# Kernel optimization log

Hardware: AMD Instinct MI355X
Metric: run time of the kernel (lower is better)

Reference implementation:

```python
import jax, jax.numpy as jnp
import numpy as np

N_E, E_DIM, BETA = 8192, 512, 0.25


def setup_inputs() -> dict:
    key = jax.random.key(0)
    k1, k2 = jax.random.split(key)
    z = jax.random.normal(k1, (16, 1024, E_DIM), dtype=jnp.float32)
    # embedding initialized uniform(-1/n_e, 1/n_e)
    emb_w = jax.random.uniform(k2, (N_E, E_DIM), dtype=jnp.float32,
                               minval=-1.0 / N_E, maxval=1.0 / N_E)
    return {"z": z, "emb_w": emb_w}


def reference(z, emb_w):
    B, T, D = z.shape
    zf = z.reshape(-1, D)  # [BT, D]
    # squared-distance matrix: ||z||^2 + ||e||^2 - 2 z e^T  -> [BT, n_e]
    d = (jnp.sum(zf * zf, axis=1, keepdims=True)
         + jnp.sum(emb_w * emb_w, axis=1)
         - 2.0 * jnp.einsum('bd,nd->bn', zf, emb_w))
    idx = jnp.argmin(d, axis=1)  # [BT]
    z_q = emb_w[idx].reshape(z.shape)  # [B, T, D]
    # legacy=False: beta * commit + codebook term
    loss = (BETA * jnp.mean((jax.lax.stop_gradient(z_q) - z) ** 2)
            + jnp.mean((z_q - jax.lax.stop_gradient(z)) ** 2))
    # straight-through: value equals z_q
    z_q_st = z + jax.lax.stop_gradient(z_q - z)
    idx_out = idx.reshape(B, T)
    v = jnp.var(idx_out.astype(jnp.float32))
    return z_q_st, loss, idx_out, v
```

## Files before the change

### kernel.cpp

```cpp
#include <hip/hip_runtime.h>


#define BT   16384
#define DIMS 512
#define NE   8192
#define NSPLIT 8
#define NTPB (NE / NSPLIT / 128)

#define LOSS_OFF 8388608
#define IDX_OFF  8388609
#define V_OFF    8404993

#define BEST_OFF  0
#define ENORM_OFF 131072
#define SUMS_OFF  163840
#define CNT_OFF   163864

typedef __attribute__((ext_vector_type(8))) short short8;
typedef __attribute__((ext_vector_type(4))) float floatx4;

#define AS1(p) ((const __attribute__((address_space(1))) void*)(p))
#define AS3(p) ((__attribute__((address_space(3))) void*)(p))

__device__ __forceinline__ unsigned f2bf(float f) {
    unsigned u = __builtin_bit_cast(unsigned, f);
    u += 0x7FFFu + ((u >> 16) & 1u);
    return u >> 16;
}

__global__ __launch_bounds__(256) void prep_kernel(
    const float* __restrict__ z, const float* __restrict__ emb,
    ushort* __restrict__ zh, ushort* __restrict__ ehh,
    float* __restrict__ enorm, unsigned long long* __restrict__ best,
    double* __restrict__ sums, unsigned* __restrict__ counter)
{
    const int lane = threadIdx.x & 63, w = threadIdx.x >> 6;
    const int b = blockIdx.x;
    if (b < NE / 4) {
        const int row = b * 4 + w;
        const float4* p = (const float4*)(emb + (size_t)row * DIMS + lane * 8);
        float4 a = p[0], bb = p[1];
        uint4 h;
        h.x = f2bf(a.x) | (f2bf(a.y) << 16);
        h.y = f2bf(a.z) | (f2bf(a.w) << 16);
        h.z = f2bf(bb.x) | (f2bf(bb.y) << 16);
        h.w = f2bf(bb.z) | (f2bf(bb.w) << 16);
        *(uint4*)(ehh + (size_t)row * DIMS + lane * 8) = h;
        float s = a.x*a.x + a.y*a.y + a.z*a.z + a.w*a.w
                + bb.x*bb.x + bb.y*bb.y + bb.z*bb.z + bb.w*bb.w;
        #pragma unroll
        for (int off = 32; off > 0; off >>= 1) s += __shfl_down(s, off, 64);
        if (lane == 0) enorm[row] = s;
    } else {
        const int row = (b - NE / 4) * 4 + w;
        const float4* p = (const float4*)(z + (size_t)row * DIMS + lane * 8);
        float4 a = p[0], bb = p[1];
        uint4 h;
        h.x = f2bf(a.x) | (f2bf(a.y) << 16);
        h.y = f2bf(a.z) | (f2bf(a.w) << 16);
        h.z = f2bf(bb.x) | (f2bf(bb.y) << 16);
        h.w = f2bf(bb.z) | (f2bf(bb.w) << 16);
        *(uint4*)(zh + (size_t)row * DIMS + lane * 8) = h;
    }
    const int gid = b * 256 + threadIdx.x;
    if (gid < BT) best[gid] = 0xFFFFFFFFFFFFFFFFULL;
    if (gid == 0) { sums[0] = 0.0; sums[1] = 0.0; sums[2] = 0.0; *counter = 0u; }
}

__global__ __launch_bounds__(256) void argmin_mfma(
    const ushort* __restrict__ zh, const ushort* __restrict__ eh,
    const float* __restrict__ enorm, unsigned long long* __restrict__ best)
{
    __shared__ __align__(16) ushort lds[2][128][64];
    const int t = threadIdx.x;
    const int w = t >> 6, lane = t & 63;
    const int quad = lane >> 4, l15 = lane & 15;
    const int mt = blockIdx.x & 127, ns = blockIdx.x >> 7;
    const int m0 = mt * 128;
    const int wm = (w & 1) * 64, wn = (w >> 1) * 64;

    const int half = w & 1;
    const int tile = (w < 2) ? 0 : 1;
    const int srow = half * 64 + (lane >> 3);
    const int lchunk = (lane & 7) ^ ((lane >> 3) & 7);
    ushort* lb0 = &lds[tile][half * 64][0];
    const ushort* zA = zh + (size_t)m0 * DIMS;

    const int px0 = quad ^ (l15 & 7);
    const int px1 = (4 + quad) ^ (l15 & 7);

    float bs[16];
    int   bn[16];
    #pragma unroll
    for (int k = 0; k < 16; k++) { bs[k] = 3.4e38f; bn[k] = 0; }

    for (int nt = 0; nt < NTPB; nt++) {
        const int n0 = (ns * NTPB + nt) * 128;
        const ushort* gbase = (w < 2) ? zA : (eh + (size_t)n0 * DIMS);

        floatx4 acc[4][4];
        #pragma unroll
        for (int i = 0; i < 4; i++)
            #pragma unroll
            for (int j = 0; j < 4; j++)
                acc[i][j] = (floatx4){0.f, 0.f, 0.f, 0.f};

        for (int k0 = 0; k0 < DIMS; k0 += 64) {
            __syncthreads();
            #pragma unroll
            for (int c = 0; c < 8; c++) {
                const ushort* g = gbase + (size_t)(srow + c * 8) * DIMS + (k0 + lchunk * 8);
                __builtin_amdgcn_global_load_lds(AS1(g), AS3(lb0 + c * 512), 16, 0, 0);
            }
            __syncthreads();
            #pragma unroll
            for (int kk = 0; kk < 2; kk++) {
                const int px = kk ? px1 : px0;
                short8 a[4], b[4];
                #pragma unroll
                for (int i = 0; i < 4; i++)
                    a[i] = *(const short8*)&lds[0][wm + i * 16 + l15][px * 8];
                #pragma unroll
                for (int j = 0; j < 4; j++)
                    b[j] = *(const short8*)&lds[1][wn + j * 16 + l15][px * 8];
                #pragma unroll
                for (int i = 0; i < 4; i++)
                    #pragma unroll
                    for (int j = 0; j < 4; j++)
                        acc[i][j] = __builtin_amdgcn_mfma_f32_16x16x32_bf16(a[i], b[j], acc[i][j], 0, 0, 0);
            }
        }

        #pragma unroll
        for (int j = 0; j < 4; j++) {
            const int n = n0 + wn + j * 16 + l15;
            const float en = enorm[n];
            #pragma unroll
            for (int i = 0; i < 4; i++)
                #pragma unroll
                for (int r = 0; r < 4; r++) {
                    const int k = i * 4 + r;
                    float s = fmaf(-2.0f, acc[i][j][r], en);
                    if (s < bs[k]) { bs[k] = s; bn[k] = n; }
                }
        }
    }

    #pragma unroll
    for (int i = 0; i < 4; i++)
        #pragma unroll
        for (int r = 0; r < 4; r++) {
            const int k = i * 4 + r;
            unsigned su = __builtin_bit_cast(unsigned, bs[k]);
            su = (su & 0x80000000u) ? ~su : (su | 0x80000000u);
            unsigned long long key = ((unsigned long long)su << 32) | (unsigned)bn[k];
            #pragma unroll
            for (int off = 1; off < 16; off <<= 1) {
                unsigned long long o = __shfl_xor(key, off, 64);
                key = (o < key) ? o : key;
            }
            if (l15 == 0) atomicMin(&best[m0 + wm + i * 16 + quad * 4 + r], key);
        }
}

__global__ __launch_bounds__(256) void gather_loss_kernel(
    const float* __restrict__ z, const float* __restrict__ emb,
    const unsigned long long* __restrict__ best,
    float* __restrict__ out, double* __restrict__ sums, unsigned* __restrict__ counter)
{
    __shared__ int sIdx[64];
    __shared__ double red[4];
    const int t = threadIdx.x;
    const int row0 = blockIdx.x * 64;
    double myIdxSum = 0.0, myIdxSq = 0.0;
    if (t < 64) {
        int row = row0 + t;
        int idx = (int)(unsigned)(best[row] & 0xFFFFFFFFULL);
        sIdx[t] = idx;
        out[IDX_OFF + row] = (float)idx;
        myIdxSum = (double)idx;
        myIdxSq = (double)idx * (double)idx;
    }
    __syncthreads();
    double acc = 0.0;
    #pragma unroll 4
    for (int i = 0; i < 32; i++) {
        int e = i * 1024 + t * 4;
        int rl = e >> 9;
        int c = e & 511;
        int idx = sIdx[rl];
        float4 zv = *(const float4*)(z + (size_t)(row0 + rl) * DIMS + c);
        float4 ev = *(const float4*)(emb + (size_t)idx * DIMS + c);
        *(float4*)(out + (size_t)(row0 + rl) * DIMS + c) = ev;
        float dx = zv.x - ev.x, dy = zv.y - ev.y;
        float dz = zv.z - ev.z, dw = zv.w - ev.w;
        acc += (double)(dx * dx + dy * dy) + (double)(dz * dz + dw * dw);
    }
    const int lane = t & 63, wv = t >> 6;
    #pragma unroll
    for (int off = 32; off > 0; off >>= 1) {
        acc      += __shfl_down(acc, off, 64);
        myIdxSum += __shfl_down(myIdxSum, off, 64);
        myIdxSq  += __shfl_down(myIdxSq, off, 64);
    }
    if (lane == 0) red[wv] = acc;
    __syncthreads();
    if (t == 0) {
        double tot = red[0] + red[1] + red[2] + red[3];
        atomicAdd(&sums[0], tot);
        atomicAdd(&sums[1], myIdxSum);
        atomicAdd(&sums[2], myIdxSq);
        __threadfence();
        unsigned old = atomicAdd(counter, 1u);
        if (old == gridDim.x - 1) {
            __threadfence();
            double s0 = atomicAdd(&sums[0], 0.0);
            double s1 = atomicAdd(&sums[1], 0.0);
            double s2 = atomicAdd(&sums[2], 0.0);
            out[LOSS_OFF] = (float)(1.25 * s0 / (double)((size_t)BT * DIMS));
            double m = s1 / (double)BT;
            out[V_OFF] = (float)(s2 / (double)BT - m * m);
        }
    }
}

extern "C" void kernel_launch(void* const* d_in, const int* in_sizes, int n_in,
                              void* d_out, int out_size, void* d_ws, size_t ws_size,
                              hipStream_t stream) {
    const float* z = (const float*)d_in[0];
    const float* emb = (const float*)d_in[1];
    float* out = (float*)d_out;
    char* ws = (char*)d_ws;
    unsigned long long* best = (unsigned long long*)(ws + BEST_OFF);
    float* enorm  = (float*)(ws + ENORM_OFF);
    double* sums  = (double*)(ws + SUMS_OFF);
    unsigned* counter = (unsigned*)(ws + CNT_OFF);

    ushort* zh = (ushort*)out;
    ushort* ehh = zh + (size_t)BT * DIMS;

    hipLaunchKernelGGL(prep_kernel, dim3(NE / 4 + BT / 4), dim3(256), 0, stream,
                       z, emb, zh, ehh, enorm, best, sums, counter);
    hipLaunchKernelGGL(argmin_mfma, dim3(128 * NSPLIT), dim3(256), 0, stream,
                       zh, ehh, enorm, best);
    hipLaunchKernelGGL(gather_loss_kernel, dim3(BT / 64), dim3(256), 0, stream,
                       z, emb, best, out, sums, counter);
}
```

Measured before the change: 289.6 us.

## Use 32x32x16 MFMA with 128x256 tiles and MFMA-ordered LDS layout

Switches the distance GEMM from 16x16x32 to 32x32x16 bf16 MFMA and widens the block tile from 128x128 to 128x256 codebook entries, halving the split count to 4. LDS is reorganized into MFMA-fragment-ordered 32-row chunks so each lane reads its operand directly with a linear offset instead of swizzled addressing. The goal is more reuse of the A tile per load and fewer LDS reads per MFMA. The cost is more accumulator registers (launch bounds set to 2 blocks/SU) and fewer blocks in flight.

```diff
diff --git a/kernel.cpp b/kernel.cpp
--- a/kernel.cpp
+++ b/kernel.cpp
@@ -4,8 +4,9 @@
 #define BT   16384
 #define DIMS 512
 #define NE   8192
-#define NSPLIT 8
-#define NTPB (NE / NSPLIT / 128)
+#define NS   4
+#define BN   256
+#define NTPB (NE / NS / BN)
 
 #define LOSS_OFF 8388608
 #define IDX_OFF  8388609
@@ -17,7 +18,7 @@
 #define CNT_OFF   163864
 
 typedef __attribute__((ext_vector_type(8))) short short8;
-typedef __attribute__((ext_vector_type(4))) float floatx4;
+typedef __attribute__((ext_vector_type(16))) float floatx16;
 
 #define AS1(p) ((const __attribute__((address_space(1))) void*)(p))
 #define AS3(p) ((__attribute__((address_space(3))) void*)(p))
@@ -67,99 +68,114 @@
     if (gid == 0) { sums[0] = 0.0; sums[1] = 0.0; sums[2] = 0.0; *counter = 0u; }
 }
 
-__global__ __launch_bounds__(256) void argmin_mfma(
+__global__ __launch_bounds__(256, 2) void argmin_mfma(
     const ushort* __restrict__ zh, const ushort* __restrict__ eh,
     const float* __restrict__ enorm, unsigned long long* __restrict__ best)
 {
-    __shared__ __align__(16) ushort lds[2][128][64];
+    __shared__ __align__(16) ushort lds[24576];
     const int t = threadIdx.x;
     const int w = t >> 6, lane = t & 63;
-    const int quad = lane >> 4, l15 = lane & 15;
+    const int l31 = lane & 31, lh = lane >> 5;
     const int mt = blockIdx.x & 127, ns = blockIdx.x >> 7;
     const int m0 = mt * 128;
-    const int wm = (w & 1) * 64, wn = (w >> 1) * 64;
-
-    const int half = w & 1;
-    const int tile = (w < 2) ? 0 : 1;
-    const int srow = half * 64 + (lane >> 3);
-    const int lchunk = (lane & 7) ^ ((lane >> 3) & 7);
-    ushort* lb0 = &lds[tile][half * 64][0];
+    const int wm = (w & 1) * 64, wn = (w >> 1) * 128;
+    const int arb = (w & 1) * 2, brb = (w >> 1) * 4;
+
+    const size_t laneoff = (size_t)l31 * DIMS + lh * 8;
     const ushort* zA = zh + (size_t)m0 * DIMS;
 
-    const int px0 = quad ^ (l15 & 7);
-    const int px1 = (4 + quad) ^ (l15 & 7);
-
-    float bs[16];
-    int   bn[16];
+    float bs[32];
+    int   bn_[32];
     #pragma unroll
-    for (int k = 0; k < 16; k++) { bs[k] = 3.4e38f; bn[k] = 0; }
+    for (int k = 0; k < 32; k++) { bs[k] = 3.4e38f; bn_[k] = 0; }
 
     for (int nt = 0; nt < NTPB; nt++) {
-        const int n0 = (ns * NTPB + nt) * 128;
-        const ushort* gbase = (w < 2) ? zA : (eh + (size_t)n0 * DIMS);
-
-        floatx4 acc[4][4];
-        #pragma unroll
-        for (int i = 0; i < 4; i++)
+        const int n0 = (ns * NTPB + nt) * BN;
+        const ushort* eB = eh + (size_t)n0 * DIMS;
+
+        const ushort* gptr[3];
+        int ldsb[3], kkst[3];
+        #pragma unroll
+        for (int gi = 0; gi < 3; gi++) {
+            const int g = w * 3 + gi;
+            if (g < 4) {
+                gptr[gi] = zA + (size_t)(g * 32) * DIMS + laneoff;
+                ldsb[gi] = g * 512;        kkst[gi] = 4 * 512;
+            } else {
+                const int rb = g - 4;
+                gptr[gi] = eB + (size_t)(rb * 32) * DIMS + laneoff;
+                ldsb[gi] = 8192 + rb * 512; kkst[gi] = 8 * 512;
+            }
+        }
+
+        floatx16 acc[2][4];
+        #pragma unroll
+        for (int i = 0; i < 2; i++)
             #pragma unroll
             for (int j = 0; j < 4; j++)
-                acc[i][j] = (floatx4){0.f, 0.f, 0.f, 0.f};
+                #pragma unroll
+                for (int r = 0; r < 16; r++) acc[i][j][r] = 0.0f;
 
         for (int k0 = 0; k0 < DIMS; k0 += 64) {
             __syncthreads();
             #pragma unroll
-            for (int c = 0; c < 8; c++) {
-                const ushort* g = gbase + (size_t)(srow + c * 8) * DIMS + (k0 + lchunk * 8);
-                __builtin_amdgcn_global_load_lds(AS1(g), AS3(lb0 + c * 512), 16, 0, 0);
-            }
+            for (int gi = 0; gi < 3; gi++)
+                #pragma unroll
+                for (int kk = 0; kk < 4; kk++)
+                    __builtin_amdgcn_global_load_lds(AS1(gptr[gi] + k0 + kk * 16),
+                                                     AS3(&lds[ldsb[gi] + kk * kkst[gi]]),
+                                                     16, 0, 0);
             __syncthreads();
             #pragma unroll
-            for (int kk = 0; kk < 2; kk++) {
-                const int px = kk ? px1 : px0;
-                short8 a[4], b[4];
-                #pragma unroll
-                for (int i = 0; i < 4; i++)
-                    a[i] = *(const short8*)&lds[0][wm + i * 16 + l15][px * 8];
+            for (int kk = 0; kk < 4; kk++) {
+                short8 a[2], b[4];
+                #pragma unroll
+                for (int i = 0; i < 2; i++)
+                    a[i] = *(const short8*)&lds[(kk * 4 + arb + i) * 512 + lane * 8];
                 #pragma unroll
                 for (int j = 0; j < 4; j++)
-                    b[j] = *(const short8*)&lds[1][wn + j * 16 + l15][px * 8];
-                #pragma unroll
-                for (int i = 0; i < 4; i++)
+                    b[j] = *(const short8*)&lds[8192 + (kk * 8 + brb + j) * 512 + lane * 8];
+                #pragma unroll
+                for (int i = 0; i < 2; i++)
                     #pragma unroll
                     for (int j = 0; j < 4; j++)
-                        acc[i][j] = __builtin_amdgcn_mfma_f32_16x16x32_bf16(a[i], b[j], acc[i][j], 0, 0, 0);
-            }
-        }
-
-        #pragma unroll
-        for (int j = 0; j < 4; j++) {
-            const int n = n0 + wn + j * 16 + l15;
-            const float en = enorm[n];
-            #pragma unroll
-            for (int i = 0; i < 4; i++)
-                #pragma unroll
-                for (int r = 0; r < 4; r++) {
-                    const int k = i * 4 + r;
-                    float s = fmaf(-2.0f, acc[i][j][r], en);
-                    if (s < bs[k]) { bs[k] = s; bn[k] = n; }
+                        acc[i][j] = __builtin_amdgcn_mfma_f32_32x32x16_bf16(a[i], b[j], acc[i][j], 0, 0, 0);
+            }
+        }
+
+        float en[4];
+        #pragma unroll
+        for (int j = 0; j < 4; j++) en[j] = enorm[n0 + wn + j * 32 + l31];
+        #pragma unroll
+        for (int i = 0; i < 2; i++)
+            #pragma unroll
+            for (int r = 0; r < 16; r++) {
+                const int k = i * 16 + r;
+                #pragma unroll
+                for (int j = 0; j < 4; j++) {
+                    float s = fmaf(-2.0f, acc[i][j][r], en[j]);
+                    if (s < bs[k]) { bs[k] = s; bn_[k] = n0 + wn + j * 32 + l31; }
                 }
-        }
+            }
     }
 
     #pragma unroll
-    for (int i = 0; i < 4; i++)
-        #pragma unroll
-        for (int r = 0; r < 4; r++) {
-            const int k = i * 4 + r;
+    for (int i = 0; i < 2; i++)
+        #pragma unroll
+        for (int r = 0; r < 16; r++) {
+            const int k = i * 16 + r;
             unsigned su = __builtin_bit_cast(unsigned, bs[k]);
             su = (su & 0x80000000u) ? ~su : (su | 0x80000000u);
-            unsigned long long key = ((unsigned long long)su << 32) | (unsigned)bn[k];
-            #pragma unroll
-            for (int off = 1; off < 16; off <<= 1) {
+            unsigned long long key = ((unsigned long long)su << 32) | (unsigned)bn_[k];
+            #pragma unroll
+            for (int off = 1; off < 32; off <<= 1) {
                 unsigned long long o = __shfl_xor(key, off, 64);
                 key = (o < key) ? o : key;
             }
-            if (l15 == 0) atomicMin(&best[m0 + wm + i * 16 + quad * 4 + r], key);
+            if (l31 == 0) {
+                const int m = m0 + wm + i * 32 + (r & 3) + 8 * (r >> 2) + 4 * lh;
+                atomicMin(&best[m], key);
+            }
         }
 }
 
@@ -241,7 +257,7 @@
 
     hipLaunchKernelGGL(prep_kernel, dim3(NE / 4 + BT / 4), dim3(256), 0, stream,
                        z, emb, zh, ehh, enorm, best, sums, counter);
-    hipLaunchKernelGGL(argmin_mfma, dim3(128 * NSPLIT), dim3(256), 0, stream,
+    hipLaunchKernelGGL(argmin_mfma, dim3(128 * NS), dim3(256), 0, stream,
                        zh, ehh, enorm, best);
     hipLaunchKernelGGL(gather_loss_kernel, dim3(BT / 64), dim3(256), 0, stream,
                        z, emb, best, out, sums, counter);
```

Result: slower. 334.5 us (+15.5%).

## Widen MFMA N-tile to 256 with fewer splits and shrink gather blocks

Applied to the files above, without the earlier changes.

The argmin GEMM now uses 128x256 block tiles, with each wave computing a 64x128 sub-tile (4x8 MFMA accumulators). The codebook is split 4 ways instead of 8, which halves z-tile reloads and improves operand reuse per LDS load. LDS loads are redistributed across all waves, and launch bounds request 2 blocks per CU. The cost is higher register pressure (128 accumulator floats per thread) and only 512 blocks in the grid. The gather/loss kernel also processes 32 rows per block instead of 64, doubling its block count for more parallelism.

```diff
diff --git a/kernel.cpp b/kernel.cpp
--- a/kernel.cpp
+++ b/kernel.cpp
@@ -4,8 +4,9 @@
 #define BT   16384
 #define DIMS 512
 #define NE   8192
-#define NSPLIT 8
-#define NTPB (NE / NSPLIT / 128)
+#define NS   4
+#define BN   256
+#define NTPB (NE / NS / BN)
 
 #define LOSS_OFF 8388608
 #define IDX_OFF  8388609
@@ -67,72 +68,76 @@
     if (gid == 0) { sums[0] = 0.0; sums[1] = 0.0; sums[2] = 0.0; *counter = 0u; }
 }
 
-__global__ __launch_bounds__(256) void argmin_mfma(
+__global__ __launch_bounds__(256, 2) void argmin_mfma(
     const ushort* __restrict__ zh, const ushort* __restrict__ eh,
     const float* __restrict__ enorm, unsigned long long* __restrict__ best)
 {
-    __shared__ __align__(16) ushort lds[2][128][64];
+    __shared__ __align__(16) ushort lds[24576];
     const int t = threadIdx.x;
     const int w = t >> 6, lane = t & 63;
     const int quad = lane >> 4, l15 = lane & 15;
     const int mt = blockIdx.x & 127, ns = blockIdx.x >> 7;
     const int m0 = mt * 128;
-    const int wm = (w & 1) * 64, wn = (w >> 1) * 64;
-
-    const int half = w & 1;
-    const int tile = (w < 2) ? 0 : 1;
-    const int srow = half * 64 + (lane >> 3);
-    const int lchunk = (lane & 7) ^ ((lane >> 3) & 7);
-    ushort* lb0 = &lds[tile][half * 64][0];
+    const int wm = (w & 1) * 64, wn = (w >> 1) * 128;
+
+    const int l8 = lane >> 3, c8 = lane & 7;
+    const int glane = l8 * DIMS + (c8 ^ l8) * 8;
     const ushort* zA = zh + (size_t)m0 * DIMS;
+    int srcoff[12], ldso[12]; bool fromB[12];
+    #pragma unroll
+    for (int gi = 0; gi < 12; gi++) {
+        const int q = w * 12 + gi;
+        if (q < 16) { fromB[gi] = false; srcoff[gi] = q * 8 * DIMS + glane; ldso[gi] = q * 512; }
+        else { const int c = q - 16; fromB[gi] = true; srcoff[gi] = c * 8 * DIMS + glane; ldso[gi] = 8192 + c * 512; }
+    }
 
     const int px0 = quad ^ (l15 & 7);
     const int px1 = (4 + quad) ^ (l15 & 7);
 
     float bs[16];
-    int   bn[16];
-    #pragma unroll
-    for (int k = 0; k < 16; k++) { bs[k] = 3.4e38f; bn[k] = 0; }
+    int   bn_[16];
+    #pragma unroll
+    for (int k = 0; k < 16; k++) { bs[k] = 3.4e38f; bn_[k] = 0; }
 
     for (int nt = 0; nt < NTPB; nt++) {
-        const int n0 = (ns * NTPB + nt) * 128;
-        const ushort* gbase = (w < 2) ? zA : (eh + (size_t)n0 * DIMS);
-
-        floatx4 acc[4][4];
+        const int n0 = (ns * NTPB + nt) * BN;
+        const ushort* eB = eh + (size_t)n0 * DIMS;
+
+        floatx4 acc[4][8];
         #pragma unroll
         for (int i = 0; i < 4; i++)
             #pragma unroll
-            for (int j = 0; j < 4; j++)
+            for (int j = 0; j < 8; j++)
                 acc[i][j] = (floatx4){0.f, 0.f, 0.f, 0.f};
 
         for (int k0 = 0; k0 < DIMS; k0 += 64) {
             __syncthreads();
             #pragma unroll
-            for (int c = 0; c < 8; c++) {
-                const ushort* g = gbase + (size_t)(srow + c * 8) * DIMS + (k0 + lchunk * 8);
-                __builtin_amdgcn_global_load_lds(AS1(g), AS3(lb0 + c * 512), 16, 0, 0);
+            for (int gi = 0; gi < 12; gi++) {
+                const ushort* g = (fromB[gi] ? eB : zA) + srcoff[gi] + k0;
+                __builtin_amdgcn_global_load_lds(AS1(g), AS3(&lds[ldso[gi]]), 16, 0, 0);
             }
             __syncthreads();
             #pragma unroll
             for (int kk = 0; kk < 2; kk++) {
-                const int px = kk ? px1 : px0;
-                short8 a[4], b[4];
+                const int po = (kk ? px1 : px0) * 8;
+                short8 a[4], b[8];
                 #pragma unroll
                 for (int i = 0; i < 4; i++)
-                    a[i] = *(const short8*)&lds[0][wm + i * 16 + l15][px * 8];
-                #pragma unroll
-                for (int j = 0; j < 4; j++)
-                    b[j] = *(const short8*)&lds[1][wn + j * 16 + l15][px * 8];
+                    a[i] = *(const short8*)&lds[(wm + i * 16 + l15) * 64 + po];
+                #pragma unroll
+                for (int j = 0; j < 8; j++)
+                    b[j] = *(const short8*)&lds[8192 + (wn + j * 16 + l15) * 64 + po];
                 #pragma unroll
                 for (int i = 0; i < 4; i++)
                     #pragma unroll
-                    for (int j = 0; j < 4; j++)
+                    for (int j = 0; j < 8; j++)
                         acc[i][j] = __builtin_amdgcn_mfma_f32_16x16x32_bf16(a[i], b[j], acc[i][j], 0, 0, 0);
             }
         }
 
         #pragma unroll
-        for (int j = 0; j < 4; j++) {
+        for (int j = 0; j < 8; j++) {
             const int n = n0 + wn + j * 16 + l15;
             const float en = enorm[n];
             #pragma unroll
@@ -141,7 +146,7 @@
                 for (int r = 0; r < 4; r++) {
                     const int k = i * 4 + r;
                     float s = fmaf(-2.0f, acc[i][j][r], en);
-                    if (s < bs[k]) { bs[k] = s; bn[k] = n; }
+                    if (s < bs[k]) { bs[k] = s; bn_[k] = n; }
                 }
         }
     }
@@ -153,7 +158,7 @@
             const int k = i * 4 + r;
             unsigned su = __builtin_bit_cast(unsigned, bs[k]);
             su = (su & 0x80000000u) ? ~su : (su | 0x80000000u);
-            unsigned long long key = ((unsigned long long)su << 32) | (unsigned)bn[k];
+            unsigned long long key = ((unsigned long long)su << 32) | (unsigned)bn_[k];
             #pragma unroll
             for (int off = 1; off < 16; off <<= 1) {
                 unsigned long long o = __shfl_xor(key, off, 64);
@@ -168,12 +173,12 @@
     const unsigned long long* __restrict__ best,
     float* __restrict__ out, double* __restrict__ sums, unsigned* __restrict__ counter)
 {
-    __shared__ int sIdx[64];
+    __shared__ int sIdx[32];
     __shared__ double red[4];
     const int t = threadIdx.x;
-    const int row0 = blockIdx.x * 64;
+    const int row0 = blockIdx.x * 32;
     double myIdxSum = 0.0, myIdxSq = 0.0;
-    if (t < 64) {
+    if (t < 32) {
         int row = row0 + t;
         int idx = (int)(unsigned)(best[row] & 0xFFFFFFFFULL);
         sIdx[t] = idx;
@@ -184,7 +189,7 @@
     __syncthreads();
     double acc = 0.0;
     #pragma unroll 4
-    for (int i = 0; i < 32; i++) {
+    for (int i = 0; i < 16; i++) {
         int e = i * 1024 + t * 4;
         int rl = e >> 9;
         int c = e & 511;
@@ -241,8 +246,8 @@
 
     hipLaunchKernelGGL(prep_kernel, dim3(NE / 4 + BT / 4), dim3(256), 0, stream,
                        z, emb, zh, ehh, enorm, best, sums, counter);
-    hipLaunchKernelGGL(argmin_mfma, dim3(128 * NSPLIT), dim3(256), 0, stream,
+    hipLaunchKernelGGL(argmin_mfma, dim3(128 * NS), dim3(256), 0, stream,
                        zh, ehh, enorm, best);
-    hipLaunchKernelGGL(gather_loss_kernel, dim3(BT / 64), dim3(256), 0, stream,
+    hipLaunchKernelGGL(gather_loss_kernel, dim3(BT / 32), dim3(256), 0, stream,
                        z, emb, best, out, sums, counter);
 }
```

Measured after the change: 268.4 us. -7.3%, faster.
